# Kernel optimization log

Measured on AMD Instinct MI355X. Metric: run time of the kernel, lower is better.

Reference implementation:

```python
import jax, jax.numpy as jnp
import numpy as np

B, K, TOPK = 32, 8192, 1000
F, AED = 1024, 128          # state_feature_size, action_embedding_dim
E = F + AED + 1             # memory slot width = 1153
ADIM = 4672


def _gelu(x):
    return jax.nn.gelu(x, approximate=False)  # torch default GELU is exact erf


def setup_inputs() -> dict:
    key = jax.random.key(0)
    ks = jax.random.split(key, 14)
    def W(k, i, o):
        return jax.random.normal(k, (i, o), jnp.float32) / np.float32(np.sqrt(i))
    return {
        'features': jax.random.normal(ks[0], (B, F), jnp.float32),
        'memory': jax.random.normal(ks[1], (K, E), jnp.float32),
        'W1s': W(ks[2], 2 * F, 512), 'b1s': jnp.zeros(512, jnp.float32),
        'W2s': W(ks[3], 512, 1), 'b2s': jnp.zeros(1, jnp.float32),
        'W1e': W(ks[4], 2 * F, 256), 'b1e': jnp.zeros(256, jnp.float32),
        'W2e': W(ks[5], 256, 1), 'b2e': jnp.zeros(1, jnp.float32),
        'Wp1': W(ks[6], F + AED, 768), 'bp1': jnp.zeros(768, jnp.float32),
        'Wp2': W(ks[7], 768, ADIM), 'bp2': jnp.zeros(ADIM, jnp.float32),
        'Wv1': W(ks[8], F, 512), 'bv1': jnp.zeros(512, jnp.float32),
        'Wv2': W(ks[9], 512, 1), 'bv2': jnp.zeros(1, jnp.float32),
        'Wm1': W(ks[10], F, 512), 'bm1': jnp.zeros(512, jnp.float32),
        'Wm2': W(ks[11], 512, 1), 'bm2': jnp.zeros(1, jnp.float32),
    }


def reference(features, memory, W1s, b1s, W2s, b2s, W1e, b1e, W2e, b2e,
              Wp1, bp1, Wp2, bp2, Wv1, bv1, Wv2, bv2, Wm1, bm1, Wm2, bm2):
    # ---- ReadHead.StateAttention: relu(fc1(cat(q,k))) -> fc2 -> softmax over K slots.
    # fc1(cat(q,k)) = q @ W1s[:F] + k @ W1s[F:] + b : avoids materializing the (B,K,2F) concat.
    feat_mem = memory[:, :F]                                   # (K,F)
    q1 = features @ W1s[:F]                                    # (B,512)
    k1 = feat_mem @ W1s[F:]                                    # (K,512)
    h1 = jax.nn.relu(q1[:, None, :] + k1[None, :, :] + b1s)    # (B,K,512)
    scores = jnp.squeeze(h1 @ W2s, -1) + b2s                   # (B,K)
    attn_w = jax.nn.softmax(scores, axis=1)
    _, topk_idx = jax.lax.top_k(attn_w, TOPK)                  # (B,TOPK)

    # ---- retrieve_relevant_memory: batched gather of top-k slots
    rel = jnp.take(memory, topk_idx, axis=0)                   # (B,TOPK,E)
    mem_feat = rel[..., :F]
    # torch does .long() on the action slice: truncate toward zero, no grad flow
    actions = jax.lax.stop_gradient(jnp.trunc(rel[..., F:E - 1]))  # (B,TOPK,AED)
    results = rel[..., -1]                                     # (B,TOPK)

    # ---- ActionResultAttention over the TOPK retrieved slots (GELU MLP attention)
    q2 = features @ W1e[:F]                                    # (B,256)
    k2 = jnp.einsum('bkf,fh->bkh', mem_feat, W1e[F:])          # (B,TOPK,256)
    h2 = _gelu(q2[:, None, :] + k2 + b1e)
    s2 = jnp.squeeze(h2 @ W2e, -1) + b2e                       # (B,TOPK)
    w2 = jax.nn.softmax(s2, axis=1)
    weighted_actions = jnp.einsum('bka,bk->ba', actions, w2)   # (B,AED)
    weighted_results = jnp.einsum('bk,bk->b', results, w2)[:, None]  # (B,1)

    # ---- policy / value heads + ValueMLPAttention blend
    pf = jnp.concatenate([features, weighted_actions], axis=1)
    action_logits = _gelu(pf @ Wp1 + bp1) @ Wp2 + bp2          # (B,ADIM)
    board_vals = jnp.tanh(_gelu(features @ Wv1 + bv1) @ Wv2 + bv2)  # (B,1)
    aw = jax.nn.sigmoid(_gelu(features @ Wm1 + bm1) @ Wm2 + bm2)
    value_output = aw * weighted_results + (1.0 - aw) * board_vals
    return action_logits, board_vals, value_output, weighted_actions, weighted_results
```

## Files before the change

kernel.cpp:

```cpp
#include <hip/hip_runtime.h>
#include <math.h>

#define B_ 32
#define K_ 8192
#define TOPK_ 1000
#define F_ 1024
#define E_ 1153
#define H1_ 512
#define H2_ 256
#define PH_ 768
#define ADIM_ 4672

#define OFF_BV   149504
#define OFF_VAL  149536
#define OFF_WACT 149568
#define OFF_WRES 153664

typedef __attribute__((ext_vector_type(8))) short v8s;
typedef __attribute__((ext_vector_type(4))) float v4f;
typedef __attribute__((ext_vector_type(4))) unsigned short v4u16;

#define GLD16(gp, lp) __builtin_amdgcn_global_load_lds( \
    (const __attribute__((address_space(1))) void*)(gp), \
    (__attribute__((address_space(3))) void*)(lp), 16, 0, 0)

__device__ __forceinline__ float gelu_f(float x) {
  return 0.5f * x * (1.0f + erff(x * 0.70710678118654752440f));
}
__device__ __forceinline__ unsigned short f2bf(float x) {
  union { float f; unsigned u; } v; v.f = x;
  unsigned r = v.u + 0x7fffu + ((v.u >> 16) & 1u);
  return (unsigned short)(r >> 16);
}
__device__ __forceinline__ float bf2f(unsigned short h) {
  union { unsigned u; float f; } v; v.u = ((unsigned)h) << 16; return v.f;
}

__global__ __launch_bounds__(256) void k_split_mem(
    const float* __restrict__ memory, unsigned short* __restrict__ Ahi,
    unsigned short* __restrict__ Alo) {
  const int r = blockIdx.x;
  const int tid = threadIdx.x;
  const float* src = memory + (size_t)r * E_;
#pragma unroll
  for (int i = 0; i < 4; ++i) {
    const float x = src[tid + 256 * i];
    const unsigned short h = f2bf(x);
    Ahi[(size_t)r * 1024 + tid + 256 * i] = h;
    Alo[(size_t)r * 1024 + tid + 256 * i] = f2bf(x - bf2f(h));
  }
}

__global__ __launch_bounds__(256) void k_split_w(
    const float* __restrict__ W1s, const float* __restrict__ W1e,
    unsigned short* __restrict__ B1hi, unsigned short* __restrict__ B1lo,
    unsigned short* __restrict__ B2hi) {
  __shared__ float t[32][33];
  const int x = threadIdx.x, y = threadIdx.y;
  const int j0 = blockIdx.x * 32, k0 = blockIdx.y * 32;
#pragma unroll
  for (int i = 0; i < 4; ++i) {
    const int k = k0 + y + 8 * i;
    const int j = j0 + x;
    t[y + 8 * i][x] = (j < 512) ? W1s[(size_t)(F_ + k) * H1_ + j]
                                : W1e[(size_t)(F_ + k) * H2_ + (j - 512)];
  }
  __syncthreads();
#pragma unroll
  for (int i = 0; i < 4; ++i) {
    const int j = j0 + y + 8 * i;
    const int k = k0 + x;
    const float v = t[x][y + 8 * i];
    const unsigned short h = f2bf(v);
    if (j < 512) {
      B1hi[(size_t)j * 1024 + k] = h;
      B1lo[(size_t)j * 1024 + k] = f2bf(v - bf2f(h));
    } else {
      B2hi[(size_t)(j - 512) * 1024 + k] = h;
    }
  }
}

__global__ __launch_bounds__(256) void k_init5(
    const float* __restrict__ b1s, const float* __restrict__ b1e,
    const float* __restrict__ bv1, const float* __restrict__ bm1,
    const float* __restrict__ bp1, float* __restrict__ q1b,
    float* __restrict__ q2b, float* __restrict__ v1h, float* __restrict__ m1h,
    float* __restrict__ hp_acc, float* __restrict__ wact,
    float* __restrict__ wres) {
  const int idx = blockIdx.x * 256 + threadIdx.x;
  if (idx < 32 * 2560) {
    const int b = idx / 2560, j = idx - b * 2560;
    if (j < 512) q1b[b * 512 + j] = b1s[j];
    else if (j < 768) q2b[b * 256 + (j - 512)] = b1e[j - 512];
    else if (j < 1280) v1h[b * 512 + (j - 768)] = bv1[j - 768];
    else if (j < 1792) m1h[b * 512 + (j - 1280)] = bm1[j - 1280];
    else hp_acc[b * 768 + (j - 1792)] = bp1[j - 1792];
  } else {
    const int k = idx - 32 * 2560;
    if (k < 4096) wact[k] = 0.f;
    else if (k < 4128) wres[k - 4096] = 0.f;
  }
}

__global__ __launch_bounds__(256) void k_batch1(
    const float* __restrict__ features, const float* __restrict__ W1s,
    const float* __restrict__ W1e, const float* __restrict__ Wv1,
    const float* __restrict__ Wm1, float* __restrict__ q1b,
    float* __restrict__ q2b, float* __restrict__ v1h,
    float* __restrict__ m1h) {
  const int t = blockIdx.x, kc0 = blockIdx.y * 128;
  const float* Wp; float* Cp; int ldw, n0;
  if (t < 8)       { Wp = W1s; Cp = q1b; ldw = 512; n0 = t * 64; }
  else if (t < 12) { Wp = W1e; Cp = q2b; ldw = 256; n0 = (t - 8) * 64; }
  else if (t < 20) { Wp = Wv1; Cp = v1h; ldw = 512; n0 = (t - 12) * 64; }
  else             { Wp = Wm1; Cp = m1h; ldw = 512; n0 = (t - 20) * 64; }
  const int col = n0 + (threadIdx.x & 63);
  const int r0 = __builtin_amdgcn_readfirstlane((int)(threadIdx.x >> 6)) * 8;
  const float* A = features + (size_t)r0 * F_ + kc0;
  float acc[8] = {0.f, 0.f, 0.f, 0.f, 0.f, 0.f, 0.f, 0.f};
  for (int k = 0; k < 128; ++k) {
    const float w = Wp[(size_t)(kc0 + k) * ldw + col];
#pragma unroll
    for (int r = 0; r < 8; ++r) acc[r] = fmaf(A[r * F_ + k], w, acc[r]);
  }
#pragma unroll
  for (int r = 0; r < 8; ++r)
    atomicAdd(&Cp[(size_t)(r0 + r) * ldw + col], acc[r]);
}

__device__ __forceinline__ void stage80(
    const unsigned short* __restrict__ src, int row_base, int k0,
    char* lds, int lds_off, int nchunks, int tid) {
  for (int i = 0; i * 256 < nchunks; ++i) {
    const int c = i * 256 + tid;
    if (c < nchunks) {
      const int row = c / 5, sub = c % 5;
      const int s = (sub == 4) ? 0 : sub;
      const unsigned short* g = src + (size_t)(row_base + row) * 1024 + k0 + s * 8;
      GLD16(g, lds + lds_off + i * 4096 + ((tid >> 6) * 1024));
    }
  }
}

__global__ __launch_bounds__(256) void k_gemm1(
    const unsigned short* __restrict__ Ahi, const unsigned short* __restrict__ Alo,
    const unsigned short* __restrict__ B1hi, const unsigned short* __restrict__ B1lo,
    float* __restrict__ C1) {
  __shared__ unsigned short lds[15360];
  char* L = (char*)lds;
  const int tid = threadIdx.x;
  const int lane = tid & 63, w = tid >> 6;
  const int m0 = blockIdx.x * 128;
  const int n0 = blockIdx.y * 64;
  const int wr = w >> 1, wc = w & 1;
  v4f acc[4][2];
#pragma unroll
  for (int mi = 0; mi < 4; ++mi)
#pragma unroll
    for (int ni = 0; ni < 2; ++ni) acc[mi][ni] = (v4f)(0.f);

  for (int k0 = 0; k0 < 1024; k0 += 32) {
    __syncthreads();
    stage80(Ahi, m0, k0, L, 0, 640, tid);
    stage80(Alo, m0, k0, L, 10240, 640, tid);
    stage80(B1hi, n0, k0, L, 20480, 320, tid);
    stage80(B1lo, n0, k0, L, 25600, 320, tid);
    asm volatile("s_waitcnt vmcnt(0)" ::: "memory");
    __syncthreads();
    v8s ah[4], al[4], bh[2], bl[2];
    const int fo = (lane >> 4) * 16;
#pragma unroll
    for (int mi = 0; mi < 4; ++mi) {
      const int ro = (wr * 64 + mi * 16 + (lane & 15)) * 80 + fo;
      ah[mi] = *(const v8s*)(L + ro);
      al[mi] = *(const v8s*)(L + 10240 + ro);
    }
#pragma unroll
    for (int ni = 0; ni < 2; ++ni) {
      const int ro = (wc * 32 + ni * 16 + (lane & 15)) * 80 + fo;
      bh[ni] = *(const v8s*)(L + 20480 + ro);
      bl[ni] = *(const v8s*)(L + 25600 + ro);
    }
#pragma unroll
    for (int mi = 0; mi < 4; ++mi)
#pragma unroll
      for (int ni = 0; ni < 2; ++ni) {
        acc[mi][ni] = __builtin_amdgcn_mfma_f32_16x16x32_bf16(ah[mi], bh[ni], acc[mi][ni], 0, 0, 0);
        acc[mi][ni] = __builtin_amdgcn_mfma_f32_16x16x32_bf16(ah[mi], bl[ni], acc[mi][ni], 0, 0, 0);
        acc[mi][ni] = __builtin_amdgcn_mfma_f32_16x16x32_bf16(al[mi], bh[ni], acc[mi][ni], 0, 0, 0);
      }
  }
#pragma unroll
  for (int mi = 0; mi < 4; ++mi)
#pragma unroll
    for (int ni = 0; ni < 2; ++ni)
#pragma unroll
      for (int j = 0; j < 4; ++j) {
        const int mrow = m0 + wr * 64 + mi * 16 + (lane >> 4) * 4 + j;
        const int ncol = n0 + wc * 32 + ni * 16 + (lane & 15);
        C1[(size_t)mrow * 512 + ncol] = acc[mi][ni][j];
      }
}

__global__ __launch_bounds__(256) void k_gemm2(
    const unsigned short* __restrict__ Ahi, const unsigned short* __restrict__ B2hi,
    unsigned short* __restrict__ C2) {
  __shared__ unsigned short lds[7680];
  char* L = (char*)lds;
  const int tid = threadIdx.x;
  const int lane = tid & 63, w = tid >> 6;
  const int m0 = blockIdx.x * 128;
  const int n0 = blockIdx.y * 64;
  const int wr = w >> 1, wc = w & 1;
  v4f acc[4][2];
#pragma unroll
  for (int mi = 0; mi < 4; ++mi)
#pragma unroll
    for (int ni = 0; ni < 2; ++ni) acc[mi][ni] = (v4f)(0.f);

  for (int k0 = 0; k0 < 1024; k0 += 32) {
    __syncthreads();
    stage80(Ahi, m0, k0, L, 0, 640, tid);
    stage80(B2hi, n0, k0, L, 10240, 320, tid);
    asm volatile("s_waitcnt vmcnt(0)" ::: "memory");
    __syncthreads();
    v8s ah[4], bh[2];
    const int fo = (lane >> 4) * 16;
#pragma unroll
    for (int mi = 0; mi < 4; ++mi)
      ah[mi] = *(const v8s*)(L + (wr * 64 + mi * 16 + (lane & 15)) * 80 + fo);
#pragma unroll
    for (int ni = 0; ni < 2; ++ni)
      bh[ni] = *(const v8s*)(L + 10240 + (wc * 32 + ni * 16 + (lane & 15)) * 80 + fo);
#pragma unroll
    for (int mi = 0; mi < 4; ++mi)
#pragma unroll
      for (int ni = 0; ni < 2; ++ni)
        acc[mi][ni] = __builtin_amdgcn_mfma_f32_16x16x32_bf16(ah[mi], bh[ni], acc[mi][ni], 0, 0, 0);
  }
#pragma unroll
  for (int mi = 0; mi < 4; ++mi)
#pragma unroll
    for (int ni = 0; ni < 2; ++ni)
#pragma unroll
      for (int j = 0; j < 4; ++j) {
        const int mrow = m0 + wr * 64 + mi * 16 + (lane >> 4) * 4 + j;
        const int ncol = n0 + wc * 32 + ni * 16 + (lane & 15);
        C2[(size_t)mrow * 256 + ncol] = f2bf(acc[mi][ni][j]);
      }
}

__global__ __launch_bounds__(256) void k_scores2(
    const float* __restrict__ C1, const float* __restrict__ q1b,
    const float* __restrict__ W2s, const float* __restrict__ b2s,
    float* __restrict__ scores) {
  __shared__ float4 c4[8 * 129];
  __shared__ float4 w4[128];
  const int tid = threadIdx.x;
  const int kbase = blockIdx.x * 8;
#pragma unroll
  for (int p = 0; p < 4; ++p) {
    const int idx = p * 256 + tid;
    const int row = idx >> 7, c = idx & 127;
    c4[row * 129 + c] = *(const float4*)&C1[(size_t)(kbase + row) * 512 + c * 4];
  }
  if (tid < 128) w4[tid] = *(const float4*)&W2s[tid * 4];
  __syncthreads();
  const int b = tid >> 3, ks = tid & 7;
  const float4* qrow = (const float4*)&q1b[b * 512];
  float acc = 0.f;
  for (int i = 0; i < 128; ++i) {
    const float4 c = c4[ks * 129 + i];
    const float4 q = qrow[i];
    const float4 w = w4[i];
    acc += fmaxf(q.x + c.x, 0.f) * w.x + fmaxf(q.y + c.y, 0.f) * w.y +
           fmaxf(q.z + c.z, 0.f) * w.z + fmaxf(q.w + c.w, 0.f) * w.w;
  }
  scores[(size_t)b * K_ + kbase + ks] = acc + b2s[0];
}

__global__ __launch_bounds__(1024) void k_topk(
    const float* __restrict__ scores, int* __restrict__ topk_idx) {
  __shared__ unsigned key[K_];
  __shared__ unsigned whist[16][256];
  __shared__ unsigned sfx[256];
  __shared__ int eqlist[1024];
  __shared__ unsigned ctl[4];
  const int tid = threadIdx.x;
  const int wid = tid >> 6;
  const int b = blockIdx.x;
  const float* row = scores + (size_t)b * K_;
  for (int i = tid; i < K_; i += 1024) {
    const unsigned u = __float_as_uint(row[i]);
    key[i] = (u & 0x80000000u) ? ~u : (u | 0x80000000u);
  }
  unsigned prefix = 0;
  int r = TOPK_;
  for (int p = 0; p < 4; ++p) {
    const int shift = 24 - 8 * p;
    for (int i = tid; i < 16 * 256; i += 1024) ((unsigned*)whist)[i] = 0;
    __syncthreads();
    const unsigned pmask = (p == 0) ? 0u : (0xFFFFFFFFu << (shift + 8));
    for (int i = tid; i < K_; i += 1024) {
      const unsigned k = key[i];
      if ((k & pmask) == prefix) atomicAdd(&whist[wid][(k >> shift) & 255u], 1u);
    }
    __syncthreads();
    if (tid < 256) {
      unsigned s = 0;
#pragma unroll
      for (int ww = 0; ww < 16; ++ww) s += whist[ww][tid];
      sfx[tid] = s;
    }
    __syncthreads();
    for (int off = 1; off < 256; off <<= 1) {
      unsigned v = 0;
      if (tid < 256) { v = sfx[tid]; if (tid + off < 256) v += sfx[tid + off]; }
      __syncthreads();
      if (tid < 256) sfx[tid] = v;
      __syncthreads();
    }
    if (tid < 256) {
      const int Sge = (int)sfx[tid];
      const int Sgt = (tid < 255) ? (int)sfx[tid + 1] : 0;
      if (Sgt < r && r <= Sge) { ctl[0] = (unsigned)tid; ctl[1] = (unsigned)(r - Sgt); }
    }
    __syncthreads();
    prefix |= ctl[0] << shift;
    r = (int)ctl[1];
    __syncthreads();
  }
  const unsigned T = prefix;
  const int take_eq = r;
  if (tid == 0) { ctl[2] = 0; ctl[3] = 0; }
  __syncthreads();
  int* outp = topk_idx + b * TOPK_;
  for (int i = tid; i < K_; i += 1024) {
    const unsigned k = key[i];
    if (k > T) outp[atomicAdd(&ctl[2], 1u)] = i;
    else if (k == T) { const unsigned e = atomicAdd(&ctl[3], 1u); if (e < 1024) eqlist[e] = i; }
  }
  __syncthreads();
  const int m = (ctl[3] < 1024u) ? (int)ctl[3] : 1024;
  const int ngt = TOPK_ - take_eq;
  for (int sel = 0; sel < take_eq; ++sel) {
    key[tid] = (tid < m) ? (unsigned)eqlist[tid] : 0xFFFFFFFFu;
    __syncthreads();
    for (int s = 512; s > 0; s >>= 1) {
      if (tid < s) key[tid] = min(key[tid], key[tid + s]);
      __syncthreads();
    }
    const unsigned mn = key[0];
    if (tid < m && (unsigned)eqlist[tid] == mn) eqlist[tid] = 0x7FFFFFFF;
    if (tid == 0) outp[ngt + sel] = (int)mn;
    __syncthreads();
  }
}

__global__ __launch_bounds__(256) void k_s2(
    const unsigned short* __restrict__ C2, const float* __restrict__ q2b,
    const int* __restrict__ topk_idx, const float* __restrict__ W2e,
    const float* __restrict__ b2e, float* __restrict__ s2) {
  const int tid = threadIdx.x;
  const int ln = tid & 63;
  const int e = blockIdx.x * 4 + (tid >> 6);
  const int b = e / TOPK_;
  const int idx = topk_idx[e];
  const v4u16 kv = *(const v4u16*)(C2 + (size_t)idx * H2_ + ln * 4);
  const float4 qv = *(const float4*)(q2b + b * H2_ + ln * 4);
  float s = gelu_f(qv.x + bf2f(kv[0])) * W2e[ln * 4 + 0]
          + gelu_f(qv.y + bf2f(kv[1])) * W2e[ln * 4 + 1]
          + gelu_f(qv.z + bf2f(kv[2])) * W2e[ln * 4 + 2]
          + gelu_f(qv.w + bf2f(kv[3])) * W2e[ln * 4 + 3];
#pragma unroll
  for (int off = 32; off > 0; off >>= 1) s += __shfl_down(s, off);
  if (ln == 0) s2[e] = s + b2e[0];
}

__global__ __launch_bounds__(256) void k_soft(
    const float* __restrict__ s2, float* __restrict__ w2) {
  __shared__ float red[256];
  const int tid = threadIdx.x, b = blockIdx.x;
  float m = -3.4e38f;
  for (int t = tid; t < TOPK_; t += 256) m = fmaxf(m, s2[b * TOPK_ + t]);
  red[tid] = m;
  __syncthreads();
  for (int s = 128; s > 0; s >>= 1) {
    if (tid < s) red[tid] = fmaxf(red[tid], red[tid + s]);
    __syncthreads();
  }
  m = red[0];
  __syncthreads();
  float ps = 0.f;
  for (int t = tid; t < TOPK_; t += 256) {
    const float ev = expf(s2[b * TOPK_ + t] - m);
    w2[b * TOPK_ + t] = ev;
    ps += ev;
  }
  red[tid] = ps;
  __syncthreads();
  for (int s = 128; s > 0; s >>= 1) {
    if (tid < s) red[tid] += red[tid + s];
    __syncthreads();
  }
  const float inv = 1.f / red[0];
  for (int t = tid; t < TOPK_; t += 256) w2[b * TOPK_ + t] *= inv;
}

__global__ __launch_bounds__(256) void k_weighted(
    const int* __restrict__ topk_idx, const float* __restrict__ w2,
    const float* __restrict__ memory, float* __restrict__ wact_acc,
    float* __restrict__ wres_acc) {
  const int blk = blockIdx.x;
  const int b = blk >> 3, c = blk & 7;
  const int tid = threadIdx.x;
  const int g = tid >> 7, a = tid & 127;
  float acc = 0.f, accr = 0.f;
  for (int t = c * 125 + g; t < (c + 1) * 125; t += 2) {
    const int idx = topk_idx[b * TOPK_ + t];
    const float wv = w2[b * TOPK_ + t];
    acc += truncf(memory[(size_t)idx * E_ + F_ + a]) * wv;
    if (a == 0) accr += wv * memory[(size_t)idx * E_ + (E_ - 1)];
  }
  atomicAdd(&wact_acc[b * 128 + a], acc);
  if (a == 0) atomicAdd(&wres_acc[b], accr);
}

__global__ __launch_bounds__(512) void k_value_epi(
    const float* __restrict__ v1h, const float* __restrict__ m1h,
    const float* __restrict__ Wv2, const float* __restrict__ bv2,
    const float* __restrict__ Wm2, const float* __restrict__ bm2,
    float* __restrict__ aw, float* __restrict__ out) {
  __shared__ float red[512];
  const int tid = threadIdx.x, b = blockIdx.x, net = blockIdx.y;
  const float* h = net ? m1h : v1h;
  const float* W2 = net ? Wm2 : Wv2;
  red[tid] = gelu_f(h[b * 512 + tid]) * W2[tid];
  __syncthreads();
  for (int s = 256; s > 0; s >>= 1) {
    if (tid < s) red[tid] += red[tid + s];
    __syncthreads();
  }
  if (tid == 0) {
    const float v = red[0] + (net ? bm2[0] : bv2[0]);
    if (net == 0) out[OFF_BV + b] = tanhf(v);
    else aw[b] = 1.f / (1.f + expf(-v));
  }
}

__global__ __launch_bounds__(256) void k_hp2(
    const float* __restrict__ features, const float* __restrict__ wact,
    const float* __restrict__ Wp1, float* __restrict__ hp_acc) {
  const int kc0 = blockIdx.y * 128;
  const int col = blockIdx.x * 64 + (threadIdx.x & 63);
  const int r0 = __builtin_amdgcn_readfirstlane((int)(threadIdx.x >> 6)) * 8;
  const float* A; int lda;
  if (blockIdx.y == 8) { A = wact + (size_t)r0 * 128; lda = 128; }
  else { A = features + (size_t)r0 * F_ + kc0; lda = F_; }
  float acc[8] = {0.f, 0.f, 0.f, 0.f, 0.f, 0.f, 0.f, 0.f};
  for (int k = 0; k < 128; ++k) {
    const float w = Wp1[(size_t)(kc0 + k) * PH_ + col];
#pragma unroll
    for (int r = 0; r < 8; ++r) acc[r] = fmaf(A[r * lda + k], w, acc[r]);
  }
#pragma unroll
  for (int r = 0; r < 8; ++r)
    atomicAdd(&hp_acc[(size_t)(r0 + r) * PH_ + col], acc[r]);
}

__global__ void k_gelu_ip(float* __restrict__ p, int n) {
  const int i = blockIdx.x * 256 + threadIdx.x;
  if (i < n) p[i] = gelu_f(p[i]);
}

__global__ __launch_bounds__(256) void k_logits_init(
    const float* __restrict__ bp2, float* __restrict__ out) {
  const int i = blockIdx.x * 256 + threadIdx.x;
  if (i < B_ * ADIM_) out[i] = bp2[i % ADIM_];
}

__global__ __launch_bounds__(256) void k_logits2(
    const float* __restrict__ hp, const float* __restrict__ Wp2,
    float* __restrict__ out) {
  const int kc0 = blockIdx.y * 256;
  const int col = blockIdx.x * 64 + (threadIdx.x & 63);
  const int r0 = __builtin_amdgcn_readfirstlane((int)(threadIdx.x >> 6)) * 8;
  const float* A = hp + (size_t)r0 * PH_ + kc0;
  float acc[8] = {0.f, 0.f, 0.f, 0.f, 0.f, 0.f, 0.f, 0.f};
  for (int k = 0; k < 256; ++k) {
    const float w = Wp2[(size_t)(kc0 + k) * ADIM_ + col];
#pragma unroll
    for (int r = 0; r < 8; ++r) acc[r] = fmaf(A[r * PH_ + k], w, acc[r]);
  }
#pragma unroll
  for (int r = 0; r < 8; ++r)
    atomicAdd(&out[(size_t)(r0 + r) * ADIM_ + col], acc[r]);
}

__global__ __launch_bounds__(256) void k_finalize(
    const float* __restrict__ wact, const float* __restrict__ wres,
    const float* __restrict__ aw, float* __restrict__ out) {
  const int i = blockIdx.x * 256 + threadIdx.x;
  if (i < 4096) {
    out[OFF_WACT + i] = wact[i];
  } else if (i < 4128) {
    const int b = i - 4096;
    out[OFF_WRES + b] = wres[b];
    const float A = aw[b];
    out[OFF_VAL + b] = A * wres[b] + (1.f - A) * out[OFF_BV + b];
  }
}

extern "C" void kernel_launch(void* const* d_in, const int* in_sizes, int n_in,
                              void* d_out, int out_size, void* d_ws,
                              size_t ws_size, hipStream_t stream) {
  (void)in_sizes; (void)n_in; (void)out_size; (void)ws_size;
  const float* features = (const float*)d_in[0];
  const float* memory   = (const float*)d_in[1];
  const float* W1s = (const float*)d_in[2];
  const float* b1s = (const float*)d_in[3];
  const float* W2s = (const float*)d_in[4];
  const float* b2s = (const float*)d_in[5];
  const float* W1e = (const float*)d_in[6];
  const float* b1e = (const float*)d_in[7];
  const float* W2e = (const float*)d_in[8];
  const float* b2e = (const float*)d_in[9];
  const float* Wp1 = (const float*)d_in[10];
  const float* bp1 = (const float*)d_in[11];
  const float* Wp2 = (const float*)d_in[12];
  const float* bp2 = (const float*)d_in[13];
  const float* Wv1 = (const float*)d_in[14];
  const float* bv1 = (const float*)d_in[15];
  const float* Wv2 = (const float*)d_in[16];
  const float* bv2 = (const float*)d_in[17];
  const float* Wm1 = (const float*)d_in[18];
  const float* bm1 = (const float*)d_in[19];
  const float* Wm2 = (const float*)d_in[20];
  const float* bm2 = (const float*)d_in[21];
  float* out = (float*)d_out;

  char* W = (char*)d_ws;
  unsigned short* Ahi  = (unsigned short*)(W);
  unsigned short* Alo  = (unsigned short*)(W + (16u << 20));
  unsigned short* B1hi = (unsigned short*)(W + (32u << 20));
  unsigned short* B1lo = (unsigned short*)(W + (33u << 20));
  unsigned short* B2hi = (unsigned short*)(W + (34u << 20));
  float*          C1   = (float*)(W + (35u << 20));
  unsigned short* C2   = (unsigned short*)(W + (51u << 20));
  float*          scores = (float*)(W + (55u << 20));
  char* S = W + (56u << 20);
  float* q1b      = (float*)(S);
  float* q2b      = (float*)(S + 65536);
  float* s2       = (float*)(S + 98304);
  float* w2       = (float*)(S + 226304);
  int*   topk     = (int*)  (S + 354304);
  float* wact_acc = (float*)(S + 482304);
  float* wres_acc = (float*)(S + 498688);
  float* aw       = (float*)(S + 498816);
  float* hp_acc   = (float*)(S + 498944);
  float* v1h      = (float*)(S + 597248);
  float* m1h      = (float*)(S + 662784);

  k_split_mem<<<8192, 256, 0, stream>>>(memory, Ahi, Alo);
  k_split_w<<<dim3(24, 32), dim3(32, 8), 0, stream>>>(W1s, W1e, B1hi, B1lo, B2hi);
  k_init5<<<337, 256, 0, stream>>>(b1s, b1e, bv1, bm1, bp1, q1b, q2b, v1h, m1h,
                                   hp_acc, wact_acc, wres_acc);
  k_batch1<<<dim3(28, 8), 256, 0, stream>>>(features, W1s, W1e, Wv1, Wm1,
                                            q1b, q2b, v1h, m1h);
  k_gemm1<<<dim3(64, 8), 256, 0, stream>>>(Ahi, Alo, B1hi, B1lo, C1);
  k_gemm2<<<dim3(64, 4), 256, 0, stream>>>(Ahi, B2hi, C2);
  k_scores2<<<1024, 256, 0, stream>>>(C1, q1b, W2s, b2s, scores);
  k_topk<<<32, 1024, 0, stream>>>(scores, topk);
  k_s2<<<8000, 256, 0, stream>>>(C2, q2b, topk, W2e, b2e, s2);
  k_soft<<<32, 256, 0, stream>>>(s2, w2);
  k_weighted<<<256, 256, 0, stream>>>(topk, w2, memory, wact_acc, wres_acc);
  k_value_epi<<<dim3(32, 2), 512, 0, stream>>>(v1h, m1h, Wv2, bv2, Wm2, bm2, aw, out);
  k_hp2<<<dim3(12, 9), 256, 0, stream>>>(features, wact_acc, Wp1, hp_acc);
  k_gelu_ip<<<96, 256, 0, stream>>>(hp_acc, B_ * PH_);
  k_logits_init<<<584, 256, 0, stream>>>(bp2, out);
  k_logits2<<<dim3(73, 3), 256, 0, stream>>>(hp_acc, Wp2, out);
  k_finalize<<<17, 256, 0, stream>>>(wact_acc, wres_acc, aw, out);
}
```

Measured before the change: 389.9 us.

## Replace skinny batch GEMMs with LDS-staged 32-row register-tiled kernel

Introduces a shared skinny-GEMM body that stages a 32x64 activation tile in LDS and has each thread compute all 32 rows for two adjacent columns. Weights are read once per K-slice with float2 loads instead of once per 8-row group. This replaces the batch1, hp2 and logits kernels. The features half of the Wp1 projection is also moved off the critical path by launching it early, leaving only the small weighted-actions part after the memory read. The cost is heavy register pressure from 64 accumulators per thread, smaller 128-thread blocks, and more atomics per thread.

```diff
diff --git a/kernel.cpp b/kernel.cpp
--- a/kernel.cpp
+++ b/kernel.cpp
@@ -103,30 +103,90 @@
   }
 }
 
-__global__ __launch_bounds__(256) void k_batch1(
+__device__ __forceinline__ void skinny32_body(
+    const float* __restrict__ A, int lda, int kbase,
+    const float* __restrict__ Wp, int ldw, int n0, int N,
+    float* __restrict__ C, int ldc, float* __restrict__ lA) {
+  const int tid = threadIdx.x;
+#pragma unroll
+  for (int j = 0; j < 16; ++j) {
+    const int idx = j * 128 + tid;
+    const int r = idx >> 6, k = idx & 63;
+    lA[k * 36 + r] = A[(size_t)r * lda + kbase + k];
+  }
+  __syncthreads();
+  const int c0 = n0 + tid * 2;
+  if (c0 >= N) return;
+  float acc[32][2];
+#pragma unroll
+  for (int r = 0; r < 32; ++r) { acc[r][0] = 0.f; acc[r][1] = 0.f; }
+  const float* wp = Wp + (size_t)kbase * ldw + c0;
+#pragma unroll 2
+  for (int k = 0; k < 64; ++k) {
+    const float2 w = *(const float2*)&wp[(size_t)k * ldw];
+#pragma unroll
+    for (int rq = 0; rq < 8; ++rq) {
+      const float4 a = *(const float4*)&lA[k * 36 + rq * 4];
+      acc[rq * 4 + 0][0] = fmaf(a.x, w.x, acc[rq * 4 + 0][0]);
+      acc[rq * 4 + 0][1] = fmaf(a.x, w.y, acc[rq * 4 + 0][1]);
+      acc[rq * 4 + 1][0] = fmaf(a.y, w.x, acc[rq * 4 + 1][0]);
+      acc[rq * 4 + 1][1] = fmaf(a.y, w.y, acc[rq * 4 + 1][1]);
+      acc[rq * 4 + 2][0] = fmaf(a.z, w.x, acc[rq * 4 + 2][0]);
+      acc[rq * 4 + 2][1] = fmaf(a.z, w.y, acc[rq * 4 + 2][1]);
+      acc[rq * 4 + 3][0] = fmaf(a.w, w.x, acc[rq * 4 + 3][0]);
+      acc[rq * 4 + 3][1] = fmaf(a.w, w.y, acc[rq * 4 + 3][1]);
+    }
+  }
+#pragma unroll
+  for (int r = 0; r < 32; ++r) {
+    atomicAdd(&C[(size_t)r * ldc + c0], acc[r][0]);
+    atomicAdd(&C[(size_t)r * ldc + c0 + 1], acc[r][1]);
+  }
+}
+
+__global__ __launch_bounds__(128) void k_skinny_batch1(
     const float* __restrict__ features, const float* __restrict__ W1s,
     const float* __restrict__ W1e, const float* __restrict__ Wv1,
     const float* __restrict__ Wm1, float* __restrict__ q1b,
     float* __restrict__ q2b, float* __restrict__ v1h,
     float* __restrict__ m1h) {
-  const int t = blockIdx.x, kc0 = blockIdx.y * 128;
+  __shared__ float lA[64 * 36];
+  const int t = blockIdx.x;
   const float* Wp; float* Cp; int ldw, n0;
-  if (t < 8)       { Wp = W1s; Cp = q1b; ldw = 512; n0 = t * 64; }
-  else if (t < 12) { Wp = W1e; Cp = q2b; ldw = 256; n0 = (t - 8) * 64; }
-  else if (t < 20) { Wp = Wv1; Cp = v1h; ldw = 512; n0 = (t - 12) * 64; }
-  else             { Wp = Wm1; Cp = m1h; ldw = 512; n0 = (t - 20) * 64; }
-  const int col = n0 + (threadIdx.x & 63);
-  const int r0 = __builtin_amdgcn_readfirstlane((int)(threadIdx.x >> 6)) * 8;
-  const float* A = features + (size_t)r0 * F_ + kc0;
-  float acc[8] = {0.f, 0.f, 0.f, 0.f, 0.f, 0.f, 0.f, 0.f};
-  for (int k = 0; k < 128; ++k) {
-    const float w = Wp[(size_t)(kc0 + k) * ldw + col];
-#pragma unroll
-    for (int r = 0; r < 8; ++r) acc[r] = fmaf(A[r * F_ + k], w, acc[r]);
-  }
-#pragma unroll
-  for (int r = 0; r < 8; ++r)
-    atomicAdd(&Cp[(size_t)(r0 + r) * ldw + col], acc[r]);
+  switch (t) {
+    case 0: Wp = W1s; Cp = q1b; ldw = 512; n0 = 0;   break;
+    case 1: Wp = W1s; Cp = q1b; ldw = 512; n0 = 256; break;
+    case 2: Wp = W1e; Cp = q2b; ldw = 256; n0 = 0;   break;
+    case 3: Wp = Wv1; Cp = v1h; ldw = 512; n0 = 0;   break;
+    case 4: Wp = Wv1; Cp = v1h; ldw = 512; n0 = 256; break;
+    case 5: Wp = Wm1; Cp = m1h; ldw = 512; n0 = 0;   break;
+    default: Wp = Wm1; Cp = m1h; ldw = 512; n0 = 256; break;
+  }
+  skinny32_body(features, F_, blockIdx.y * 64, Wp, ldw, n0, ldw, Cp, ldw, lA);
+}
+
+__global__ __launch_bounds__(128) void k_skinny_hp_feat(
+    const float* __restrict__ features, const float* __restrict__ Wp1,
+    float* __restrict__ hp_acc) {
+  __shared__ float lA[64 * 36];
+  skinny32_body(features, F_, blockIdx.y * 64, Wp1, PH_, blockIdx.x * 256, PH_,
+                hp_acc, PH_, lA);
+}
+
+__global__ __launch_bounds__(128) void k_skinny_hp_wact(
+    const float* __restrict__ wact, const float* __restrict__ Wp1,
+    float* __restrict__ hp_acc) {
+  __shared__ float lA[64 * 36];
+  skinny32_body(wact, 128, blockIdx.y * 64, Wp1 + (size_t)F_ * PH_, PH_,
+                blockIdx.x * 256, PH_, hp_acc, PH_, lA);
+}
+
+__global__ __launch_bounds__(128) void k_skinny_logits(
+    const float* __restrict__ hp, const float* __restrict__ Wp2,
+    float* __restrict__ out) {
+  __shared__ float lA[64 * 36];
+  skinny32_body(hp, PH_, blockIdx.y * 64, Wp2, ADIM_, blockIdx.x * 256, ADIM_,
+                out, ADIM_, lA);
 }
 
 __device__ __forceinline__ void stage80(
@@ -449,26 +509,6 @@
   }
 }
 
-__global__ __launch_bounds__(256) void k_hp2(
-    const float* __restrict__ features, const float* __restrict__ wact,
-    const float* __restrict__ Wp1, float* __restrict__ hp_acc) {
-  const int kc0 = blockIdx.y * 128;
-  const int col = blockIdx.x * 64 + (threadIdx.x & 63);
-  const int r0 = __builtin_amdgcn_readfirstlane((int)(threadIdx.x >> 6)) * 8;
-  const float* A; int lda;
-  if (blockIdx.y == 8) { A = wact + (size_t)r0 * 128; lda = 128; }
-  else { A = features + (size_t)r0 * F_ + kc0; lda = F_; }
-  float acc[8] = {0.f, 0.f, 0.f, 0.f, 0.f, 0.f, 0.f, 0.f};
-  for (int k = 0; k < 128; ++k) {
-    const float w = Wp1[(size_t)(kc0 + k) * PH_ + col];
-#pragma unroll
-    for (int r = 0; r < 8; ++r) acc[r] = fmaf(A[r * lda + k], w, acc[r]);
-  }
-#pragma unroll
-  for (int r = 0; r < 8; ++r)
-    atomicAdd(&hp_acc[(size_t)(r0 + r) * PH_ + col], acc[r]);
-}
-
 __global__ void k_gelu_ip(float* __restrict__ p, int n) {
   const int i = blockIdx.x * 256 + threadIdx.x;
   if (i < n) p[i] = gelu_f(p[i]);
@@ -478,24 +518,6 @@
     const float* __restrict__ bp2, float* __restrict__ out) {
   const int i = blockIdx.x * 256 + threadIdx.x;
   if (i < B_ * ADIM_) out[i] = bp2[i % ADIM_];
-}
-
-__global__ __launch_bounds__(256) void k_logits2(
-    const float* __restrict__ hp, const float* __restrict__ Wp2,
-    float* __restrict__ out) {
-  const int kc0 = blockIdx.y * 256;
-  const int col = blockIdx.x * 64 + (threadIdx.x & 63);
-  const int r0 = __builtin_amdgcn_readfirstlane((int)(threadIdx.x >> 6)) * 8;
-  const float* A = hp + (size_t)r0 * PH_ + kc0;
-  float acc[8] = {0.f, 0.f, 0.f, 0.f, 0.f, 0.f, 0.f, 0.f};
-  for (int k = 0; k < 256; ++k) {
-    const float w = Wp2[(size_t)(kc0 + k) * ADIM_ + col];
-#pragma unroll
-    for (int r = 0; r < 8; ++r) acc[r] = fmaf(A[r * PH_ + k], w, acc[r]);
-  }
-#pragma unroll
-  for (int r = 0; r < 8; ++r)
-    atomicAdd(&out[(size_t)(r0 + r) * ADIM_ + col], acc[r]);
 }
 
 __global__ __launch_bounds__(256) void k_finalize(
@@ -566,8 +588,9 @@
   k_split_w<<<dim3(24, 32), dim3(32, 8), 0, stream>>>(W1s, W1e, B1hi, B1lo, B2hi);
   k_init5<<<337, 256, 0, stream>>>(b1s, b1e, bv1, bm1, bp1, q1b, q2b, v1h, m1h,
                                    hp_acc, wact_acc, wres_acc);
-  k_batch1<<<dim3(28, 8), 256, 0, stream>>>(features, W1s, W1e, Wv1, Wm1,
-                                            q1b, q2b, v1h, m1h);
+  k_skinny_batch1<<<dim3(7, 16), 128, 0, stream>>>(features, W1s, W1e, Wv1, Wm1,
+                                                   q1b, q2b, v1h, m1h);
+  k_skinny_hp_feat<<<dim3(3, 16), 128, 0, stream>>>(features, Wp1, hp_acc);
   k_gemm1<<<dim3(64, 8), 256, 0, stream>>>(Ahi, Alo, B1hi, B1lo, C1);
   k_gemm2<<<dim3(64, 4), 256, 0, stream>>>(Ahi, B2hi, C2);
   k_scores2<<<1024, 256, 0, stream>>>(C1, q1b, W2s, b2s, scores);
@@ -575,10 +598,10 @@
   k_s2<<<8000, 256, 0, stream>>>(C2, q2b, topk, W2e, b2e, s2);
   k_soft<<<32, 256, 0, stream>>>(s2, w2);
   k_weighted<<<256, 256, 0, stream>>>(topk, w2, memory, wact_acc, wres_acc);
+  k_skinny_hp_wact<<<dim3(3, 2), 128, 0, stream>>>(wact_acc, Wp1, hp_acc);
+  k_gelu_ip<<<96, 256, 0, stream>>>(hp_acc, B_ * PH_);
   k_value_epi<<<dim3(32, 2), 512, 0, stream>>>(v1h, m1h, Wv2, bv2, Wm2, bm2, aw, out);
-  k_hp2<<<dim3(12, 9), 256, 0, stream>>>(features, wact_acc, Wp1, hp_acc);
-  k_gelu_ip<<<96, 256, 0, stream>>>(hp_acc, B_ * PH_);
   k_logits_init<<<584, 256, 0, stream>>>(bp2, out);
-  k_logits2<<<dim3(73, 3), 256, 0, stream>>>(hp_acc, Wp2, out);
+  k_skinny_logits<<<dim3(19, 12), 128, 0, stream>>>(hp_acc, Wp2, out);
   k_finalize<<<17, 256, 0, stream>>>(wact_acc, wres_acc, aw, out);
 }
```

After: 370.2 us. 5.1% less time.
